# Kernel tuning notes

Measured on AMD Instinct MI355X. Metric: run time of the kernel, lower is better.

Reference implementation:

```python
import jax, jax.numpy as jnp
import numpy as np

B, S, H, M, E = 64, 512, 1024, 26, 676  # batch, seq, hidden, max_nodes, max_edges (M*M)


def setup_inputs() -> dict:
    key = jax.random.key(0)
    ks = jax.random.split(key, 16)
    seq = jax.random.normal(ks[0], (B, S, H), jnp.float32)
    # ragged, strictly-increasing sentence-end offsets in [1, S-1], zero-padded tail
    rng = np.random.RandomState(0)
    off = np.zeros((B, M - 1), np.int64)
    for b in range(B):
        c = rng.randint(5, M)  # count of valid offsets per sample (ragged)
        off[b, :c] = np.sort(rng.choice(np.arange(1, S), size=c, replace=False))
    s = 1.0 / np.sqrt(H)
    s3 = 1.0 / np.sqrt(3 * H)
    return {
        'sequence_outputs': seq,
        'proof_offsets': jnp.asarray(off),
        'node_labels': jax.random.randint(ks[1], (B, M), 0, 2),
        'edge_labels': jax.random.randint(ks[2], (B, E), 0, 2),
        'W_naf': jax.random.normal(ks[3], (H, H), jnp.float32) * s,
        'b_naf': jnp.zeros((H,), jnp.float32),
        'W_cd': jax.random.normal(ks[4], (H, H), jnp.float32) * s,
        'b_cd': jnp.zeros((H,), jnp.float32),
        'W_co': jax.random.normal(ks[5], (H, 2), jnp.float32) * s,
        'b_co': jnp.zeros((2,), jnp.float32),
        'W_nd': jax.random.normal(ks[6], (H, H), jnp.float32) * s,
        'b_nd': jnp.zeros((H,), jnp.float32),
        'W_no': jax.random.normal(ks[7], (H, 2), jnp.float32) * s,
        'b_no': jnp.zeros((2,), jnp.float32),
        'W_ed': jax.random.normal(ks[8], (3 * H, H), jnp.float32) * s3,
        'b_ed': jnp.zeros((H,), jnp.float32),
        'W_eo': jax.random.normal(ks[9], (H, 2), jnp.float32) * s,
        'b_eo': jnp.zeros((2,), jnp.float32),
    }


def reference(sequence_outputs, proof_offsets, node_labels, edge_labels,
              W_naf, b_naf, W_cd, b_cd, W_co, b_co,
              W_nd, b_nd, W_no, b_no, W_ed, b_ed, W_eo, b_eo):
    Bx, Sx, Hx = sequence_outputs.shape
    Mx = node_labels.shape[1]
    Ex = edge_labels.shape[1]

    cls = sequence_outputs[:, 0, :]                       # [B,H]
    naf = cls @ W_naf + b_naf                             # NAF node embedding
    logits = jnp.tanh(cls @ W_cd + b_cd) @ W_co + b_co    # RobertaClassificationHead (eval: dropout=id)

    # segment-mean pooling via inclusive prefix sums: segment j = tokens (prev_j, off_j]
    P = jnp.cumsum(sequence_outputs, axis=1)              # [B,S,H]
    off = proof_offsets                                   # [B,M-1]
    prev = jnp.concatenate([jnp.zeros((Bx, 1), off.dtype), off[:, :-1]], axis=1)
    valid = off > 0                                       # [B,M-1]
    seg_sum = (jnp.take_along_axis(P, off[..., None], axis=1)
               - jnp.take_along_axis(P, prev[..., None], axis=1))  # [B,M-1,H]
    seg_len = jnp.maximum(off - prev, 1).astype(sequence_outputs.dtype)
    seg_mean = seg_sum / seg_len[..., None] * valid[..., None]

    count = valid.sum(axis=1)                             # nodes per sample (excl. NAF)
    # node embeddings: seg means at 0..count-1, NAF at index count, zeros after
    node_full = jnp.concatenate([seg_mean, jnp.zeros((Bx, 1, Hx), seg_mean.dtype)], axis=1)  # [B,M,H]
    idx = jnp.arange(Mx)
    node_full = node_full + (idx[None, :, None] == count[:, None, None]) * naf[:, None, :]

    # all-pairs edge features over n=count+1 nodes, row-major flat k=i*n+j, zero-padded to E
    n = count + 1                                         # [B]
    k = jnp.arange(Ex)                                    # [E]
    i = jnp.clip(k[None, :] // n[:, None], 0, Mx - 1)     # [B,E]
    j = jnp.clip(k[None, :] % n[:, None], 0, Mx - 1)
    valid_e = (k[None, :] < (n * n)[:, None])[..., None]
    ni = jnp.take_along_axis(node_full, i[..., None], axis=1)  # [B,E,H]
    nj = jnp.take_along_axis(node_full, j[..., None], axis=1)
    edge = jnp.concatenate([nj, ni, nj - ni], axis=-1) * valid_e  # [B,E,3H]

    node_logits = jnp.tanh(node_full @ W_nd + b_nd) @ W_no + b_no
    edge_logits = jnp.tanh(edge @ W_ed + b_ed) @ W_eo + b_eo
    return (logits, node_logits, edge_logits)
```

## Files before the change

### kernel.cpp

```cpp
#include <hip/hip_runtime.h>
#include <hip/hip_bf16.h>

#define B_ 64
#define S_ 512
#define H_ 1024
#define M_ 26
#define E_ 676

typedef short bf16x8 __attribute__((ext_vector_type(8)));
typedef float f32x4 __attribute__((ext_vector_type(4)));

__device__ __forceinline__ void gload16(const void* g, void* l) {
    __builtin_amdgcn_global_load_lds((const __attribute__((address_space(1))) unsigned int*)g,
                                     (__attribute__((address_space(3))) unsigned int*)l,
                                     16, 0, 0);
}

__device__ __forceinline__ float tanh_fast(float x) {
    float e = __expf(2.0f * x);
    return 1.0f - 2.0f * __builtin_amdgcn_rcpf(e + 1.0f);
}

__global__ __launch_bounds__(256) void k_stage1(
    const float* __restrict__ seq, const int* __restrict__ off,
    const float* __restrict__ Wnaf, const float* __restrict__ Wcd,
    const float* __restrict__ Wnd, const float* __restrict__ Wed,
    const float* __restrict__ bed, const float* __restrict__ Weo,
    const float* __restrict__ beo, const float* __restrict__ bnd,
    const float* __restrict__ Wno, const float* __restrict__ bno,
    __hip_bfloat16* __restrict__ Wt, int* __restrict__ count,
    int* __restrict__ base, int* __restrict__ rowmap,
    float* __restrict__ econ, float* __restrict__ nconst,
    float* __restrict__ naf8, float* __restrict__ cdh8,
    __hip_bfloat16* __restrict__ nodeB) {
    __shared__ __attribute__((aligned(16))) char smraw[20992];
    int bid = blockIdx.x;
    int tid = threadIdx.x;

    if (bid < 256) {
        __hip_bfloat16 (*ldsB)[40] = (__hip_bfloat16(*)[40])smraw;
        int* offs_s = (int*)(smraw + 20480);
        float* invL = (float*)(smraw + 20608);
        int b = bid >> 2, h0 = (bid & 3) * 256;
        int w = tid >> 6, l = tid & 63;

        if (tid < M_ - 1) offs_s[tid] = off[b * (M_ - 1) + tid];
        __syncthreads();
        int c = 0;
        while (c < M_ - 1 && offs_s[c] > 0) c++;
        int offmax = offs_s[c - 1];
        if (tid < 32)
            invL[tid] = (tid < c) ? 1.0f / (float)(offs_s[tid] - (tid ? offs_s[tid - 1] : 0))
                                  : 0.0f;
        int row0 = (l & 15), row1 = 16 + (l & 15);
        int offm0 = (row0 < c) ? offs_s[row0] : 0;
        int prv0  = (offm0 > 0) ? (row0 ? offs_s[row0 - 1] : 0) : 1;
        int offm1 = (row1 < c) ? offs_s[row1] : 0;
        int prv1  = (offm1 > 0) ? offs_s[row1 - 1] : 1;

        int nkt = (offmax >> 5) + 1;
        const float* sb = seq + (size_t)b * S_ * H_ + h0;
        float4 rg[8];
#pragma unroll
        for (int i = 0; i < 2; ++i)
#pragma unroll
            for (int r = 0; r < 4; ++r)
                rg[i * 4 + r] = *(const float4*)(sb + (size_t)((i * 4 + w) * 4 + r) * H_ + 4 * l);
        f32x4 acc[2][4] = {};
        int tA = (l >> 4) * 8;

        for (int kt = 0; kt < nkt; ++kt) {
            asm volatile("s_waitcnt vmcnt(0)" ::: "memory");
            ushort4 pk[2][4];
#pragma unroll
            for (int i = 0; i < 2; ++i)
#pragma unroll
                for (int q = 0; q < 4; ++q) {
                    float f0 = (q==0)?rg[i*4+0].x:(q==1)?rg[i*4+0].y:(q==2)?rg[i*4+0].z:rg[i*4+0].w;
                    float f1 = (q==0)?rg[i*4+1].x:(q==1)?rg[i*4+1].y:(q==2)?rg[i*4+1].z:rg[i*4+1].w;
                    float f2 = (q==0)?rg[i*4+2].x:(q==1)?rg[i*4+2].y:(q==2)?rg[i*4+2].z:rg[i*4+2].w;
                    float f3 = (q==0)?rg[i*4+3].x:(q==1)?rg[i*4+3].y:(q==2)?rg[i*4+3].z:rg[i*4+3].w;
                    __hip_bfloat16 __attribute__((aligned(8))) hh[4] = {
                        __float2bfloat16(f0), __float2bfloat16(f1),
                        __float2bfloat16(f2), __float2bfloat16(f3)};
                    pk[i][q] = *(const ushort4*)hh;
                }
            if (kt + 1 < nkt) {
#pragma unroll
                for (int i = 0; i < 2; ++i)
#pragma unroll
                    for (int r = 0; r < 4; ++r) {
                        int tl = (kt + 1) * 32 + (i * 4 + w) * 4 + r;
                        rg[i * 4 + r] = *(const float4*)(sb + (size_t)tl * H_ + 4 * l);
                    }
                __builtin_amdgcn_sched_barrier(0);
            }
#pragma unroll
            for (int i = 0; i < 2; ++i)
#pragma unroll
                for (int q = 0; q < 4; ++q)
                    *(ushort4*)&ldsB[4 * l + q][(i * 4 + w) * 4] = pk[i][q];
            asm volatile("s_waitcnt lgkmcnt(0)" ::: "memory");
            __builtin_amdgcn_s_barrier();
            int T0 = kt * 32;
            bf16x8 af0, af1;
#pragma unroll
            for (int i = 0; i < 8; ++i) {
                int t = T0 + tA + i;
                af0[i] = (t > prv0 && t <= offm0) ? (short)0x3F80 : (short)0;
                af1[i] = (t > prv1 && t <= offm1) ? (short)0x3F80 : (short)0;
            }
#pragma unroll
            for (int nn = 0; nn < 4; ++nn) {
                bf16x8 bfr = *(const bf16x8*)&ldsB[(w * 4 + nn) * 16 + (l & 15)][tA];
                acc[0][nn] = __builtin_amdgcn_mfma_f32_16x16x32_bf16(af0, bfr, acc[0][nn], 0, 0, 0);
                acc[1][nn] = __builtin_amdgcn_mfma_f32_16x16x32_bf16(af1, bfr, acc[1][nn], 0, 0, 0);
            }
            __builtin_amdgcn_s_barrier();
        }
#pragma unroll
        for (int mt = 0; mt < 2; ++mt)
#pragma unroll
            for (int nn = 0; nn < 4; ++nn) {
                f32x4 v = acc[mt][nn];
                int hcol = h0 + (w * 4 + nn) * 16 + (l & 15);
#pragma unroll
                for (int r = 0; r < 4; ++r) {
                    int m = mt * 16 + (l >> 4) * 4 + r;
                    if (m < c)
                        nodeB[((size_t)(b * M_ + m)) * H_ + hcol] =
                            __float2bfloat16(v[r] * invL[m]);
                }
            }
    } else if (bid < 512) {
        float* smem = (float*)smraw;
        float (*As)[64] = (float(*)[64])smem;
        float (*Bs)[64] = (float(*)[64])(smem + 1024);
        int e = bid - 256;
        int bx = e & 31;
        int kg = e >> 5;
        int kbase = kg * 128;
        const float* W;
        float* dst;
        int cbase;
        if (bx < 16) { W = Wnaf; dst = naf8 + (size_t)kg * 64 * H_; cbase = bx * 64; }
        else         { W = Wcd;  dst = cdh8 + (size_t)kg * 64 * H_; cbase = (bx - 16) * 64; }
        int tx = tid % 16, ty = tid / 16;
        float c[4][4] = {};
        int la_row = tid / 4;
        int la_k4  = (tid % 4) * 4;
        int lb_k   = tid / 16;
        int lb_c4  = (tid % 16) * 4;
        for (int k0 = 0; k0 < 128; k0 += 16) {
            float4 a = *(const float4*)(seq + (size_t)la_row * S_ * H_ + kbase + k0 + la_k4);
            *(float4*)(&Bs[lb_k][lb_c4]) =
                *(const float4*)(W + (size_t)(kbase + k0 + lb_k) * H_ + cbase + lb_c4);
            As[la_k4 + 0][la_row] = a.x;
            As[la_k4 + 1][la_row] = a.y;
            As[la_k4 + 2][la_row] = a.z;
            As[la_k4 + 3][la_row] = a.w;
            __syncthreads();
#pragma unroll
            for (int kk = 0; kk < 16; ++kk) {
                float4 av = *(const float4*)(&As[kk][ty * 4]);
                float4 bv = *(const float4*)(&Bs[kk][tx * 4]);
                c[0][0] += av.x * bv.x; c[0][1] += av.x * bv.y; c[0][2] += av.x * bv.z; c[0][3] += av.x * bv.w;
                c[1][0] += av.y * bv.x; c[1][1] += av.y * bv.y; c[1][2] += av.y * bv.z; c[1][3] += av.y * bv.w;
                c[2][0] += av.z * bv.x; c[2][1] += av.z * bv.y; c[2][2] += av.z * bv.z; c[2][3] += av.z * bv.w;
                c[3][0] += av.w * bv.x; c[3][1] += av.w * bv.y; c[3][2] += av.w * bv.z; c[3][3] += av.w * bv.w;
            }
            __syncthreads();
        }
#pragma unroll
        for (int i = 0; i < 4; ++i) {
            float4 v = make_float4(c[i][0], c[i][1], c[i][2], c[i][3]);
            *(float4*)(dst + (size_t)(ty * 4 + i) * H_ + cbase + tx * 4) = v;
        }
    } else if (bid < 3584) {
        float (*T)[33] = (float(*)[33])smraw;
        int idx = bid - 512;
        int s = idx >> 10, rem = idx & 1023;
        int bx = rem & 31, by = rem >> 5;
        int c = tid & 31, r0 = tid >> 5;
        const int HH = H_ * H_;
#pragma unroll
        for (int i = 0; i < 4; ++i) {
            int r = r0 + 8 * i;
            size_t k = by * 32 + r, n = bx * 32 + c;
            float v;
            if (s == 0)      v = Wnd[k * H_ + n];
            else if (s == 1) v = Wed[k * H_ + n] + Wed[2 * HH + k * H_ + n];
            else             v = Wed[HH + k * H_ + n] - Wed[2 * HH + k * H_ + n];
            T[r][c] = v;
        }
        __syncthreads();
#pragma unroll
        for (int i = 0; i < 4; ++i) {
            int rr = r0 + 8 * i;
            Wt[(size_t)(s * H_ + bx * 32 + rr) * H_ + by * 32 + c] = __float2bfloat16(T[c][rr]);
        }
    } else if (bid == 3584) {
        int* cnt_s = (int*)smraw;
        int* base_s = (int*)smraw + 64;
        if (tid < 64) {
            int b = tid, c = 0;
            for (int m = 0; m < M_ - 1; ++m) c += (off[b * (M_ - 1) + m] > 0) ? 1 : 0;
            cnt_s[b] = c; count[b] = c;
        }
        __syncthreads();
        if (tid == 0) {
            int a = 0;
            for (int b = 0; b < 64; ++b) { base_s[b] = a; a += cnt_s[b] + 1; }
            base_s[64] = a;
        }
        __syncthreads();
        if (tid < 65) base[tid] = base_s[tid];
        if (tid < 64) {
            int b = tid, bs = base_s[b];
            for (int m = 0; m <= cnt_s[b]; ++m) rowmap[bs + m] = b * M_ + m;
        }
    } else {
        float* s0 = (float*)smraw; float* s1 = (float*)smraw + 256;
        float a0 = 0.f, a1 = 0.f;
        for (int h = tid; h < H_; h += 256) {
            float t = tanh_fast(bed[h]);
            a0 += t * Weo[h * 2 + 0];
            a1 += t * Weo[h * 2 + 1];
        }
        s0[tid] = a0; s1[tid] = a1; __syncthreads();
        for (int o = 128; o > 0; o >>= 1) {
            if (tid < o) { s0[tid] += s0[tid + o]; s1[tid] += s1[tid + o]; }
            __syncthreads();
        }
        if (tid == 0) { econ[0] = s0[0] + beo[0]; econ[1] = s1[0] + beo[1]; }
        __syncthreads();
        a0 = 0.f; a1 = 0.f;
        for (int h = tid; h < H_; h += 256) {
            float t = tanh_fast(bnd[h]);
            a0 += t * Wno[h * 2 + 0];
            a1 += t * Wno[h * 2 + 1];
        }
        s0[tid] = a0; s1[tid] = a1; __syncthreads();
        for (int o = 128; o > 0; o >>= 1) {
            if (tid < o) { s0[tid] += s0[tid + o]; s1[tid] += s1[tid + o]; }
            __syncthreads();
        }
        if (tid == 0) { nconst[0] = s0[0] + bno[0]; nconst[1] = s1[0] + bno[1]; }
    }
}

__global__ __launch_bounds__(256) void k_stage2s(
    const float* __restrict__ naf8, const float* __restrict__ cdh8,
    const float* __restrict__ bnaf, const int* __restrict__ count,
    __hip_bfloat16* __restrict__ nodeB,
    const float* __restrict__ bcd, const float* __restrict__ Wco,
    const float* __restrict__ bco, float* __restrict__ out) {
    __shared__ float smem[512];
    int bid = blockIdx.x;
    int tid = threadIdx.x;
    if (bid < 64) {
        int b = bid, cnt = count[b];
        float4 a = make_float4(0.f, 0.f, 0.f, 0.f);
#pragma unroll
        for (int kg = 0; kg < 8; ++kg) {
            float4 s = ((const float4*)(naf8 + (size_t)kg * 64 * H_ + (size_t)b * H_))[tid];
            a.x += s.x; a.y += s.y; a.z += s.z; a.w += s.w;
        }
        float4 bb = ((const float4*)bnaf)[tid];
        __hip_bfloat16 __attribute__((aligned(8))) h[4] = {
            __float2bfloat16(a.x + bb.x), __float2bfloat16(a.y + bb.y),
            __float2bfloat16(a.z + bb.z), __float2bfloat16(a.w + bb.w)};
        *(ushort4*)(nodeB + ((size_t)(b * M_ + cnt)) * H_ + tid * 4) = *(const ushort4*)h;
    } else {
        int b = bid - 64;
        float* s0 = smem; float* s1 = smem + 256;
        float a0 = 0.f, a1 = 0.f;
        for (int h = tid; h < H_; h += 256) {
            float v = 0.f;
#pragma unroll
            for (int kg = 0; kg < 8; ++kg) v += cdh8[(size_t)kg * 64 * H_ + (size_t)b * H_ + h];
            float t = tanh_fast(v + bcd[h]);
            a0 += t * Wco[h * 2 + 0];
            a1 += t * Wco[h * 2 + 1];
        }
        s0[tid] = a0; s1[tid] = a1; __syncthreads();
        for (int o = 128; o > 0; o >>= 1) {
            if (tid < o) { s0[tid] += s0[tid + o]; s1[tid] += s1[tid + o]; }
            __syncthreads();
        }
        if (tid == 0) { out[b * 2 + 0] = s0[0] + bco[0]; out[b * 2 + 1] = s1[0] + bco[1]; }
    }
}

#define GM 1664
#define GN 3072
#define GK 1024
__global__ __launch_bounds__(256) void k_mfma(const __hip_bfloat16* __restrict__ A,
                                              const __hip_bfloat16* __restrict__ Bt,
                                              float* __restrict__ C,
                                              const int* __restrict__ rowmap,
                                              const int* __restrict__ base) {
    __shared__ __hip_bfloat16 As[128 * 32];
    __shared__ __hip_bfloat16 Bs[128 * 32];
    int rowtotal = base[64];
    int row0 = blockIdx.y * 128;
    if (row0 >= rowtotal) return;
    int tid = threadIdx.x;
    int wid = tid >> 6, ln = tid & 63;
    int col0 = blockIdx.x * 128;
    int ai0 = row0 + wid * 16 + (ln >> 2);      if (ai0 > rowtotal - 1) ai0 = rowtotal - 1;
    int ai1 = row0 + 64 + wid * 16 + (ln >> 2); if (ai1 > rowtotal - 1) ai1 = rowtotal - 1;
    const __hip_bfloat16* ga0 = A + (size_t)rowmap[ai0] * GK + (ln & 3) * 8;
    const __hip_bfloat16* ga1 = A + (size_t)rowmap[ai1] * GK + (ln & 3) * 8;
    const __hip_bfloat16* gb = Bt + (size_t)(col0 + wid * 16 + (ln >> 2)) * GK + (ln & 3) * 8;
    __hip_bfloat16* lA = As + wid * 512;
    __hip_bfloat16* lB = Bs + wid * 512;
    int mrow = (wid >> 1) * 64, ncol = (wid & 1) * 64;
    int l15 = ln & 15, l4 = ln >> 4;
    f32x4 acc[4][4] = {};
    const __hip_bfloat16* pa = As + (size_t)(mrow + l15) * 32 + l4 * 8;
    const __hip_bfloat16* pb = Bs + (size_t)(ncol + l15) * 32 + l4 * 8;
    for (int k0 = 0; k0 < GK; k0 += 32) {
        gload16(ga0, lA);
        gload16(ga1, lA + 2048);
        gload16(gb, lB);
        gload16(gb + 64 * GK, lB + 2048);
        ga0 += 32; ga1 += 32; gb += 32;
        __syncthreads();
        bf16x8 af[4], bf[4];
#pragma unroll
        for (int mi = 0; mi < 4; ++mi) af[mi] = *(const bf16x8*)(pa + mi * 16 * 32);
#pragma unroll
        for (int ni = 0; ni < 4; ++ni) bf[ni] = *(const bf16x8*)(pb + ni * 16 * 32);
#pragma unroll
        for (int mi = 0; mi < 4; ++mi)
#pragma unroll
            for (int ni = 0; ni < 4; ++ni)
                acc[mi][ni] = __builtin_amdgcn_mfma_f32_16x16x32_bf16(af[mi], bf[ni],
                                                                      acc[mi][ni], 0, 0, 0);
        __syncthreads();
    }
#pragma unroll
    for (int mi = 0; mi < 4; ++mi)
#pragma unroll
        for (int ni = 0; ni < 4; ++ni) {
            f32x4 v = acc[mi][ni];
            int r = row0 + mrow + mi * 16 + l4 * 4;
            size_t cc = col0 + ncol + ni * 16 + l15;
#pragma unroll
            for (int j = 0; j < 4; ++j)
                if (r + j < rowtotal) C[(size_t)(r + j) * GN + cc] = v[j];
        }
}

__global__ __launch_bounds__(256) void k_stage4(
    const float* __restrict__ Cm, const int* __restrict__ count,
    const int* __restrict__ base, const float* __restrict__ bnd,
    const float* __restrict__ Wno, const float* __restrict__ bno,
    const float* __restrict__ bed, const float* __restrict__ Weo,
    const float* __restrict__ beo, const float* __restrict__ econ,
    const float* __restrict__ nconst, float* __restrict__ out_n,
    float* __restrict__ out_e) {
    int bid = blockIdx.x;
    int wid = threadIdx.x >> 6, lane = threadIdx.x & 63;
    if (bid < 416) {
        int r = bid * 4 + wid;
        int b = r / 26, m = r - b * 26;
        if (m <= count[b]) {
            const float4* src = (const float4*)(Cm + (size_t)(base[b] + m) * GN);
            float a0 = 0.f, a1 = 0.f;
#pragma unroll
            for (int it = 0; it < 4; ++it) {
                int h = lane * 4 + it * 256;
                float4 s = src[lane + it * 64];
                float4 bb = *(const float4*)(bnd + h);
                float t0 = tanh_fast(s.x + bb.x), t1 = tanh_fast(s.y + bb.y);
                float t2 = tanh_fast(s.z + bb.z), t3 = tanh_fast(s.w + bb.w);
                a0 += t0 * Wno[h * 2 + 0] + t1 * Wno[h * 2 + 2] + t2 * Wno[h * 2 + 4] + t3 * Wno[h * 2 + 6];
                a1 += t0 * Wno[h * 2 + 1] + t1 * Wno[h * 2 + 3] + t2 * Wno[h * 2 + 5] + t3 * Wno[h * 2 + 7];
            }
            for (int o = 32; o > 0; o >>= 1) { a0 += __shfl_down(a0, o); a1 += __shfl_down(a1, o); }
            if (lane == 0) { out_n[(size_t)r * 2 + 0] = a0 + bno[0]; out_n[(size_t)r * 2 + 1] = a1 + bno[1]; }
        } else if (lane == 0) {
            out_n[(size_t)r * 2 + 0] = nconst[0];
            out_n[(size_t)r * 2 + 1] = nconst[1];
        }
    } else {
        int e = bid - 416;
        int b = e >> 4;
        int wg = (e & 15) * 4 + wid;
        int n = count[b] + 1;
        int n2 = n * n;
        int bb_ = base[b];
        float4 bed4[4], w04[4], w14[4];
#pragma unroll
        for (int it = 0; it < 4; ++it) {
            int h = lane * 4 + it * 256;
            bed4[it] = *(const float4*)(bed + h);
            w04[it] = make_float4(Weo[h * 2 + 0], Weo[h * 2 + 2], Weo[h * 2 + 4], Weo[h * 2 + 6]);
            w14[it] = make_float4(Weo[h * 2 + 1], Weo[h * 2 + 3], Weo[h * 2 + 5], Weo[h * 2 + 7]);
        }
        float e0 = econ[0], e1 = econ[1];
        float b0 = beo[0], b1 = beo[1];
        for (int k = wg; k < E_; k += 64) {
            float* dst = out_e + ((size_t)b * E_ + k) * 2;
            if (k >= n2) {
                if (lane == 0) { dst[0] = e0; dst[1] = e1; }
                continue;
            }
            int i = k / n, j = k - i * n;
            const float4* U4 = (const float4*)(Cm + (size_t)(bb_ + j) * GN + H_);
            const float4* V4 = (const float4*)(Cm + (size_t)(bb_ + i) * GN + 2 * H_);
            float a0 = 0.f, a1 = 0.f;
#pragma unroll
            for (int it = 0; it < 4; ++it) {
                float4 u = U4[lane + it * 64];
                float4 v = V4[lane + it * 64];
                float t0 = tanh_fast(u.x + v.x + bed4[it].x);
                float t1 = tanh_fast(u.y + v.y + bed4[it].y);
                float t2 = tanh_fast(u.z + v.z + bed4[it].z);
                float t3 = tanh_fast(u.w + v.w + bed4[it].w);
                a0 += t0 * w04[it].x + t1 * w04[it].y + t2 * w04[it].z + t3 * w04[it].w;
                a1 += t0 * w14[it].x + t1 * w14[it].y + t2 * w14[it].z + t3 * w14[it].w;
            }
            for (int o = 32; o > 0; o >>= 1) { a0 += __shfl_down(a0, o); a1 += __shfl_down(a1, o); }
            if (lane == 0) { dst[0] = a0 + b0; dst[1] = a1 + b1; }
        }
    }
}

extern "C" void kernel_launch(void* const* d_in, const int* in_sizes, int n_in,
                              void* d_out, int out_size, void* d_ws, size_t ws_size,
                              hipStream_t stream) {
    const float* seq  = (const float*)d_in[0];
    const int*   off  = (const int*)d_in[1];
    const float* Wnaf = (const float*)d_in[4];  const float* bnaf = (const float*)d_in[5];
    const float* Wcd  = (const float*)d_in[6];  const float* bcd  = (const float*)d_in[7];
    const float* Wco  = (const float*)d_in[8];  const float* bco  = (const float*)d_in[9];
    const float* Wnd  = (const float*)d_in[10]; const float* bnd  = (const float*)d_in[11];
    const float* Wno  = (const float*)d_in[12]; const float* bno  = (const float*)d_in[13];
    const float* Wed  = (const float*)d_in[14]; const float* bed  = (const float*)d_in[15];
    const float* Weo  = (const float*)d_in[16]; const float* beo  = (const float*)d_in[17];
    float* out = (float*)d_out;

    float* ws = (float*)d_ws;
    size_t p = 0;
    float* naf8  = ws + p;  p += (size_t)8 * 64 * H_;
    float* cdh8  = ws + p;  p += (size_t)8 * 64 * H_;
    __hip_bfloat16* nodeB = (__hip_bfloat16*)(ws + p); p += (size_t)B_ * M_ * H_ / 2;
    __hip_bfloat16* Wt    = (__hip_bfloat16*)(ws + p); p += (size_t)3 * H_ * H_ / 2;
    float* Cbuf  = ws + p;  p += (size_t)GM * GN;
    int*   cnt   = (int*)(ws + p); p += 64;
    int*   base  = (int*)(ws + p); p += 65;
    int*   rowmap = (int*)(ws + p); p += GM;
    float* econ  = ws + p;  p += 2;
    float* nconst = ws + p; p += 2;


    k_stage1<<<dim3(3586), 256, 0, stream>>>(seq, off, Wnaf, Wcd, Wnd, Wed, bed, Weo, beo,
                                             bnd, Wno, bno, Wt, cnt, base, rowmap,
                                             econ, nconst, naf8, cdh8, nodeB);
    k_stage2s<<<dim3(128), 256, 0, stream>>>(naf8, cdh8, bnaf, cnt, nodeB,
                                             bcd, Wco, bco, out);
    k_mfma<<<dim3(GN / 128, GM / 128), 256, 0, stream>>>(nodeB, Wt, Cbuf, rowmap, base);
    k_stage4<<<dim3(1440), 256, 0, stream>>>(Cbuf, cnt, base, bnd, Wno, bno, bed, Weo, beo,
                                             econ, nconst,
                                             out + B_ * 2, out + B_ * 2 + B_ * M_ * 2);
}
```

Baseline: 301.5 us.

## Double-buffer MFMA GEMM with BK=64 prefetch; vectorize classifier head and edge padding

The bf16 MFMA GEMM now uses double-buffered LDS tiles with a K-step of 64. The next tile is issued via global_load_lds before computing the current one, with explicit vmcnt waits and raw s_barrier in place of __syncthreads. This is meant to hide global load latency behind MFMA work, at the cost of doubled LDS per block and fragile manual waitcnt accounting. The classifier-head reduction is also vectorized to float4 loads, and the padded edge-logit fill moves out of the per-wave loop into one coalesced block-wide store.

```diff
diff --git a/kernel.cpp b/kernel.cpp
--- a/kernel.cpp
+++ b/kernel.cpp
@@ -274,15 +274,18 @@
     } else {
         int b = bid - 64;
         float* s0 = smem; float* s1 = smem + 256;
-        float a0 = 0.f, a1 = 0.f;
-        for (int h = tid; h < H_; h += 256) {
-            float v = 0.f;
-#pragma unroll
-            for (int kg = 0; kg < 8; ++kg) v += cdh8[(size_t)kg * 64 * H_ + (size_t)b * H_ + h];
-            float t = tanh_fast(v + bcd[h]);
-            a0 += t * Wco[h * 2 + 0];
-            a1 += t * Wco[h * 2 + 1];
-        }
+        float4 a = make_float4(0.f, 0.f, 0.f, 0.f);
+#pragma unroll
+        for (int kg = 0; kg < 8; ++kg) {
+            float4 s = ((const float4*)(cdh8 + (size_t)kg * 64 * H_ + (size_t)b * H_))[tid];
+            a.x += s.x; a.y += s.y; a.z += s.z; a.w += s.w;
+        }
+        float4 bb = ((const float4*)bcd)[tid];
+        int h = tid * 4;
+        float t0 = tanh_fast(a.x + bb.x), t1 = tanh_fast(a.y + bb.y);
+        float t2 = tanh_fast(a.z + bb.z), t3 = tanh_fast(a.w + bb.w);
+        float a0 = t0 * Wco[h * 2 + 0] + t1 * Wco[h * 2 + 2] + t2 * Wco[h * 2 + 4] + t3 * Wco[h * 2 + 6];
+        float a1 = t0 * Wco[h * 2 + 1] + t1 * Wco[h * 2 + 3] + t2 * Wco[h * 2 + 5] + t3 * Wco[h * 2 + 7];
         s0[tid] = a0; s1[tid] = a1; __syncthreads();
         for (int o = 128; o > 0; o >>= 1) {
             if (tid < o) { s0[tid] += s0[tid + o]; s1[tid] += s1[tid + o]; }
@@ -300,8 +303,8 @@
                                               float* __restrict__ C,
                                               const int* __restrict__ rowmap,
                                               const int* __restrict__ base) {
-    __shared__ __hip_bfloat16 As[128 * 32];
-    __shared__ __hip_bfloat16 Bs[128 * 32];
+    __shared__ __attribute__((aligned(16))) __hip_bfloat16 As[2][2][4096];
+    __shared__ __attribute__((aligned(16))) __hip_bfloat16 Bs[2][2][4096];
     int rowtotal = base[64];
     int row0 = blockIdx.y * 128;
     if (row0 >= rowtotal) return;
@@ -312,34 +315,55 @@
     int ai1 = row0 + 64 + wid * 16 + (ln >> 2); if (ai1 > rowtotal - 1) ai1 = rowtotal - 1;
     const __hip_bfloat16* ga0 = A + (size_t)rowmap[ai0] * GK + (ln & 3) * 8;
     const __hip_bfloat16* ga1 = A + (size_t)rowmap[ai1] * GK + (ln & 3) * 8;
-    const __hip_bfloat16* gb = Bt + (size_t)(col0 + wid * 16 + (ln >> 2)) * GK + (ln & 3) * 8;
-    __hip_bfloat16* lA = As + wid * 512;
-    __hip_bfloat16* lB = Bs + wid * 512;
+    const __hip_bfloat16* gb0 = Bt + (size_t)(col0 + wid * 16 + (ln >> 2)) * GK + (ln & 3) * 8;
+    const __hip_bfloat16* gb1 = gb0 + (size_t)64 * GK;
+    int lo = wid * 512;
     int mrow = (wid >> 1) * 64, ncol = (wid & 1) * 64;
     int l15 = ln & 15, l4 = ln >> 4;
     f32x4 acc[4][4] = {};
-    const __hip_bfloat16* pa = As + (size_t)(mrow + l15) * 32 + l4 * 8;
-    const __hip_bfloat16* pb = Bs + (size_t)(ncol + l15) * 32 + l4 * 8;
-    for (int k0 = 0; k0 < GK; k0 += 32) {
-        gload16(ga0, lA);
-        gload16(ga1, lA + 2048);
-        gload16(gb, lB);
-        gload16(gb + 64 * GK, lB + 2048);
-        ga0 += 32; ga1 += 32; gb += 32;
-        __syncthreads();
-        bf16x8 af[4], bf[4];
-#pragma unroll
-        for (int mi = 0; mi < 4; ++mi) af[mi] = *(const bf16x8*)(pa + mi * 16 * 32);
-#pragma unroll
-        for (int ni = 0; ni < 4; ++ni) bf[ni] = *(const bf16x8*)(pb + ni * 16 * 32);
-#pragma unroll
-        for (int mi = 0; mi < 4; ++mi)
-#pragma unroll
-            for (int ni = 0; ni < 4; ++ni)
-                acc[mi][ni] = __builtin_amdgcn_mfma_f32_16x16x32_bf16(af[mi], bf[ni],
-                                                                      acc[mi][ni], 0, 0, 0);
-        __syncthreads();
+
+#define STAGE(buf, kt)                                                      \
+    do {                                                                    \
+        int kb_ = (kt) * 64;                                                \
+        gload16(ga0 + kb_,      &As[buf][0][0]    + lo);                    \
+        gload16(ga0 + kb_ + 32, &As[buf][1][0]    + lo);                    \
+        gload16(ga1 + kb_,      &As[buf][0][2048] + lo);                    \
+        gload16(ga1 + kb_ + 32, &As[buf][1][2048] + lo);                    \
+        gload16(gb0 + kb_,      &Bs[buf][0][0]    + lo);                    \
+        gload16(gb0 + kb_ + 32, &Bs[buf][1][0]    + lo);                    \
+        gload16(gb1 + kb_,      &Bs[buf][0][2048] + lo);                    \
+        gload16(gb1 + kb_ + 32, &Bs[buf][1][2048] + lo);                    \
+    } while (0)
+
+    STAGE(0, 0);
+    for (int kt = 0; kt < 16; ++kt) {
+        int cur = kt & 1;
+        if (kt + 1 < 16) {
+            STAGE(cur ^ 1, kt + 1);
+            asm volatile("s_waitcnt vmcnt(8)" ::: "memory");
+        } else {
+            asm volatile("s_waitcnt vmcnt(0)" ::: "memory");
+        }
+        __builtin_amdgcn_s_barrier();
+#pragma unroll
+        for (int kk = 0; kk < 2; ++kk) {
+            const __hip_bfloat16* pa = &As[cur][kk][0] + (mrow + l15) * 32 + l4 * 8;
+            const __hip_bfloat16* pb = &Bs[cur][kk][0] + (ncol + l15) * 32 + l4 * 8;
+            bf16x8 af[4], bfv[4];
+#pragma unroll
+            for (int mi = 0; mi < 4; ++mi) af[mi] = *(const bf16x8*)(pa + mi * 16 * 32);
+#pragma unroll
+            for (int ni = 0; ni < 4; ++ni) bfv[ni] = *(const bf16x8*)(pb + ni * 16 * 32);
+#pragma unroll
+            for (int mi = 0; mi < 4; ++mi)
+#pragma unroll
+                for (int ni = 0; ni < 4; ++ni)
+                    acc[mi][ni] = __builtin_amdgcn_mfma_f32_16x16x32_bf16(af[mi], bfv[ni],
+                                                                          acc[mi][ni], 0, 0, 0);
+        }
+        __builtin_amdgcn_s_barrier();
     }
+#undef STAGE
 #pragma unroll
     for (int mi = 0; mi < 4; ++mi)
 #pragma unroll
@@ -388,7 +412,8 @@
     } else {
         int e = bid - 416;
         int b = e >> 4;
-        int wg = (e & 15) * 4 + wid;
+        int blk16 = e & 15;
+        int wg = blk16 * 4 + wid;
         int n = count[b] + 1;
         int n2 = n * n;
         int bb_ = base[b];
@@ -400,14 +425,9 @@
             w04[it] = make_float4(Weo[h * 2 + 0], Weo[h * 2 + 2], Weo[h * 2 + 4], Weo[h * 2 + 6]);
             w14[it] = make_float4(Weo[h * 2 + 1], Weo[h * 2 + 3], Weo[h * 2 + 5], Weo[h * 2 + 7]);
         }
-        float e0 = econ[0], e1 = econ[1];
         float b0 = beo[0], b1 = beo[1];
-        for (int k = wg; k < E_; k += 64) {
+        for (int k = wg; k < n2; k += 64) {
             float* dst = out_e + ((size_t)b * E_ + k) * 2;
-            if (k >= n2) {
-                if (lane == 0) { dst[0] = e0; dst[1] = e1; }
-                continue;
-            }
             int i = k / n, j = k - i * n;
             const float4* U4 = (const float4*)(Cm + (size_t)(bb_ + j) * GN + H_);
             const float4* V4 = (const float4*)(Cm + (size_t)(bb_ + i) * GN + 2 * H_);
@@ -425,6 +445,12 @@
             }
             for (int o = 32; o > 0; o >>= 1) { a0 += __shfl_down(a0, o); a1 += __shfl_down(a1, o); }
             if (lane == 0) { dst[0] = a0 + b0; dst[1] = a1 + b1; }
+        }
+        if (blk16 == 0) {
+            float e0 = econ[0], e1 = econ[1];
+            float* dste = out_e + (size_t)b * E_ * 2;
+            for (int idx = 2 * n2 + (int)threadIdx.x; idx < 2 * E_; idx += 256)
+                dste[idx] = (idx & 1) ? e1 : e0;
         }
     }
 }
```

Measured after the change: 296.3 us. About the same (-1.7%).
